# Kernel tuning notes

Hardware: AMD Instinct MI355X
Metric: run time of the kernel (lower is better)

## Reference

```python
import jax
import jax.numpy as jnp
from jax import lax
import numpy as np

D_MODEL = 768
D_INNER = 1536  # d_model * expand_factor
D_STATE = 16
D_CONV = 4
BATCH = 2
SEQ = 2048
EPS = 1e-5


def silu(x):
    return x * jax.nn.sigmoid(x)


def setup_inputs() -> dict:
    key = jax.random.key(0)
    ks = jax.random.split(key, 24)
    n = lambda k, shape, s=0.1: jax.random.normal(k, shape, dtype=jnp.float32) * s
    inp = {
        "x": jax.random.normal(ks[0], (BATCH, SEQ, D_MODEL), dtype=jnp.float32),
        "ln_g": jnp.ones((D_MODEL,), jnp.float32),
        "ln_b": jnp.zeros((D_MODEL,), jnp.float32),
        "W_in": n(ks[1], (D_INNER, D_MODEL)),
        "b_in": n(ks[2], (D_INNER,)),
        "conv_w": n(ks[3], (D_INNER, 1, D_CONV), 0.02),
        "conv_b": jnp.zeros((D_INNER,), jnp.float32),
        "W_A": n(ks[4], (D_STATE, D_INNER)),
        "b_A": n(ks[5], (D_STATE,)),
        "W_B": n(ks[6], (D_STATE, D_INNER)),
        "b_B": n(ks[7], (D_STATE,)),
        "W_C": n(ks[8], (D_STATE, D_INNER)),
        "b_C": n(ks[9], (D_STATE,)),
        "W_dt": n(ks[10], (D_STATE, D_INNER)),
        "b_dt": n(ks[11], (D_STATE,)),
        "W_S": n(ks[12], (2 * D_INNER, D_INNER)),
        "b_S": n(ks[13], (2 * D_INNER,)),
        "W_gate": n(ks[14], (D_INNER, D_MODEL)),
        "b_gate": n(ks[15], (D_INNER,)),
        "W_out": n(ks[16], (D_MODEL, D_INNER)),
        "b_out": n(ks[17], (D_MODEL,)),
    }
    return inp


def reference(x, ln_g, ln_b, W_in, b_in, conv_w, conv_b, W_A, b_A, W_B, b_B,
              W_C, b_C, W_dt, b_dt, W_S, b_S, W_gate, b_gate, W_out, b_out):
    residual = x
    # LayerNorm
    mu = jnp.mean(x, axis=-1, keepdims=True)
    var = jnp.mean((x - mu) ** 2, axis=-1, keepdims=True)
    xn = (x - mu) * lax.rsqrt(var + EPS) * ln_g + ln_b
    # in projection -> [B, S, D_INNER]
    xp = xn @ W_in.T + b_in
    # depthwise causal conv1d over time
    k = conv_w.shape[-1]
    xc = jnp.moveaxis(xp, 1, 2)  # [B, D, L]
    xc = lax.conv_general_dilated(
        xc, conv_w, window_strides=(1,), padding=[(k - 1, 0)],
        dimension_numbers=("NCH", "OIH", "NCH"),
        feature_group_count=xc.shape[1])
    xc = xc + conv_b[None, :, None]
    xa = silu(jnp.moveaxis(xc, 1, 2))  # [B, S, D]
    # selective gating of SSM input (S_b computed but unused, as in source)
    S = xa @ W_S.T + b_S
    d = xa.shape[-1]
    S_a = jax.nn.sigmoid(S[..., :d])
    u = xa * S_a  # [B, S, D]
    # input-dependent SSM params [B, S, N]
    A = -jnp.exp(u @ W_A.T + b_A)
    dt = jnp.exp(u @ W_dt.T + b_dt)
    Bm = u @ W_B.T + b_B
    Cm = u @ W_C.T + b_C
    decay = jnp.exp(A * dt)  # [B, S, N]

    def step(h, inputs):
        dec_t, B_t, C_t, u_t = inputs  # [B,N],[B,N],[B,N],[B,D]
        h = h * dec_t[:, None, :] + B_t[:, None, :] * u_t[:, :, None]  # [B,D,N]
        y = jnp.einsum("bdn,bn->bd", h, C_t)
        return h, y

    h0 = jnp.zeros((u.shape[0], u.shape[2], decay.shape[-1]), u.dtype)
    scan_in = (jnp.moveaxis(decay, 1, 0), jnp.moveaxis(Bm, 1, 0),
               jnp.moveaxis(Cm, 1, 0), jnp.moveaxis(u, 1, 0))
    _, ys = lax.scan(step, h0, scan_in)
    y = jnp.moveaxis(ys, 0, 1)  # [B, S, D]
    # output gating + projection + residual
    gate = silu(xn @ W_gate.T + b_gate)
    out = (gate * y) @ W_out.T + b_out + residual
    return out
```

## Files before the change

kernel.cpp:

```cpp
#include <hip/hip_runtime.h>


typedef unsigned short u16;
using short8 = __attribute__((ext_vector_type(8))) short;
using f32x4  = __attribute__((ext_vector_type(4))) float;

#define BATCH 2
#define SEQ   2048
#define DM    768
#define DI    1536
#define NIG   (2*DI)
#define NST   16
#define LCH   64
#define NCH   32
#define NTOK  (BATCH*SEQ)

__device__ __forceinline__ u16 f2b(float x) {
  unsigned u = __float_as_uint(x);
  u += 0x7FFFu + ((u >> 16) & 1u);
  return (u16)(u >> 16);
}
__device__ __forceinline__ float b2f(u16 v) { return __uint_as_float((unsigned)v << 16); }
__device__ __forceinline__ float sigmoidf_(float x) { return 1.f / (1.f + expf(-x)); }
__device__ __forceinline__ float siluf_(float x) { return x / (1.f + expf(-x)); }

__global__ __launch_bounds__(256) void cast_bf16(const float* __restrict__ in, u16* __restrict__ out, int n4) {
  int i = blockIdx.x * 256 + threadIdx.x;
  if (i >= n4) return;
  float4 v = ((const float4*)in)[i];
  ushort4 o; o.x = f2b(v.x); o.y = f2b(v.y); o.z = f2b(v.z); o.w = f2b(v.w);
  ((ushort4*)out)[i] = o;
}

__global__ __launch_bounds__(256) void cast_ingate(const float* __restrict__ Wi, const float* __restrict__ Wg,
                                                   const float* __restrict__ bi, const float* __restrict__ bg,
                                                   u16* __restrict__ Wb, float* __restrict__ bias) {
  int i = blockIdx.x * 256 + threadIdx.x;
  if (i >= NIG * DM) return;
  int r = i / DM, c = i % DM;
  Wb[i] = f2b(r < DI ? Wi[(size_t)r * DM + c] : Wg[(size_t)(r - DI) * DM + c]);
  if (i < NIG) bias[i] = (i < DI) ? bi[i] : bg[i - DI];
}

__global__ __launch_bounds__(256) void cast_wabcd(const float* __restrict__ WA, const float* __restrict__ Wdt,
                                                  const float* __restrict__ WB, const float* __restrict__ WC,
                                                  const float* __restrict__ bA, const float* __restrict__ bdt,
                                                  const float* __restrict__ bB, const float* __restrict__ bC,
                                                  u16* __restrict__ Wb, float* __restrict__ bias64) {
  int i = blockIdx.x * 256 + threadIdx.x;
  if (i >= 64 * DI) return;
  int r = i / DI, c = i % DI;
  const float* src = (r < 16) ? WA + (size_t)r * DI
                  : (r < 32) ? Wdt + (size_t)(r - 16) * DI
                  : (r < 48) ? WB + (size_t)(r - 32) * DI
                             : WC + (size_t)(r - 48) * DI;
  Wb[i] = f2b(src[c]);
  if (i < 64) bias64[i] = (i < 16) ? bA[i] : (i < 32) ? bdt[i - 16] : (i < 48) ? bB[i - 32] : bC[i - 48];
}

__global__ __launch_bounds__(256) void ln_kernel(const float* __restrict__ x, const float* __restrict__ g,
                                                 const float* __restrict__ bb, u16* __restrict__ xn) {
  int m = blockIdx.x, tid = threadIdx.x;
  const float* xr = x + (size_t)m * DM;
  float v0 = xr[tid], v1 = xr[tid + 256], v2 = xr[tid + 512];
  float s  = v0 + v1 + v2;
  float s2 = fmaf(v0, v0, fmaf(v1, v1, v2 * v2));
  #pragma unroll
  for (int off = 32; off > 0; off >>= 1) { s += __shfl_down(s, off); s2 += __shfl_down(s2, off); }
  __shared__ float sh[8];
  int wave = tid >> 6, lane = tid & 63;
  if (lane == 0) { sh[wave] = s; sh[4 + wave] = s2; }
  __syncthreads();
  float S1 = sh[0] + sh[1] + sh[2] + sh[3];
  float S2 = sh[4] + sh[5] + sh[6] + sh[7];
  float mu = S1 * (1.f / DM);
  float var = S2 * (1.f / DM) - mu * mu;
  float rs = rsqrtf(var + 1e-5f);
  u16* o = xn + (size_t)m * DM;
  o[tid]       = f2b((v0 - mu) * rs * g[tid]       + bb[tid]);
  o[tid + 256] = f2b((v1 - mu) * rs * g[tid + 256] + bb[tid + 256]);
  o[tid + 512] = f2b((v2 - mu) * rs * g[tid + 512] + bb[tid + 512]);
}

__device__ __forceinline__ void gll16(const void* g, void* l) {
  __builtin_amdgcn_global_load_lds((const __attribute__((address_space(1))) void*)g,
                                   (__attribute__((address_space(3))) void*)l, 16, 0, 0);
}

template <int MODE>
__global__ __launch_bounds__(512) void gemm_bt(const u16* __restrict__ A, const u16* __restrict__ B,
                                               const float* __restrict__ bias, const float* __restrict__ aux,
                                               const u16* __restrict__ auxb,
                                               float* __restrict__ C, u16* __restrict__ Cb,
                                               int M, int N, int K) {
  __shared__ __align__(16) u16 As[4][128 * 32];
  __shared__ __align__(16) u16 Bs[4][128 * 32];
  const int tid = threadIdx.x, wave = tid >> 6, lane = tid & 63;

  const int nbx = gridDim.x, nwg = nbx * gridDim.y;
  const int orig = blockIdx.y * nbx + blockIdx.x;
  const int cpx = nwg >> 3;
  const int swz = (orig & 7) * cpx + (orig >> 3);
  const int m0 = (swz / nbx) * 128, n0 = (swz % nbx) * 128;

  const int wm = (wave >> 1) * 32, wn = (wave & 1) * 64;
  const int fr = lane & 15, fq = lane >> 4;
  f32x4 acc[2][4] = {};

  const int c0 = tid;
  const u16* Ag0 = A + (size_t)(m0 + (c0 >> 2)) * K + ((c0 & 3) ^ ((c0 >> 3) & 3)) * 8;
  const u16* Bg0 = B + (size_t)(n0 + (c0 >> 2)) * K + ((c0 & 3) ^ ((c0 >> 3) & 3)) * 8;
  const int lofs = (wave * 64) * 8;

  int offA[2], offB[4];
  #pragma unroll
  for (int i = 0; i < 2; ++i) {
    int ra = wm + i * 16 + fr;
    offA[i] = ra * 32 + (fq ^ ((ra >> 1) & 3)) * 8;
  }
  #pragma unroll
  for (int i = 0; i < 4; ++i) {
    int rb = wn + i * 16 + fr;
    offB[i] = rb * 32 + (fq ^ ((rb >> 1) & 3)) * 8;
  }

  const int nk = K >> 5;

#define STAGE_BT(tt) { gll16(Ag0 + (tt) * 32, (u16*)As[(tt) & 3] + lofs); \
                       gll16(Bg0 + (tt) * 32, (u16*)Bs[(tt) & 3] + lofs); }
#define COMPUTE_BT(tt) { const u16* as_ = As[(tt) & 3]; const u16* bs_ = Bs[(tt) & 3]; \
    short8 av[2], bv[4]; \
    _Pragma("unroll") for (int i = 0; i < 2; ++i) av[i] = *(const short8*)(as_ + offA[i]); \
    _Pragma("unroll") for (int i = 0; i < 4; ++i) bv[i] = *(const short8*)(bs_ + offB[i]); \
    _Pragma("unroll") for (int mi = 0; mi < 2; ++mi) \
      _Pragma("unroll") for (int ni = 0; ni < 4; ++ni) \
        acc[mi][ni] = __builtin_amdgcn_mfma_f32_16x16x32_bf16(av[mi], bv[ni], acc[mi][ni], 0, 0, 0); }

  STAGE_BT(0); STAGE_BT(1); STAGE_BT(2);

  for (int t = 0; t < nk - 3; ++t) {
    asm volatile("s_waitcnt vmcnt(4)" ::: "memory");
    __builtin_amdgcn_s_barrier();
    STAGE_BT(t + 3);
    COMPUTE_BT(t);
  }
  asm volatile("s_waitcnt vmcnt(4)" ::: "memory");
  __builtin_amdgcn_s_barrier();
  COMPUTE_BT(nk - 3);
  asm volatile("s_waitcnt vmcnt(2)" ::: "memory");
  __builtin_amdgcn_s_barrier();
  COMPUTE_BT(nk - 2);
  asm volatile("s_waitcnt vmcnt(0)" ::: "memory");
  __builtin_amdgcn_s_barrier();
  COMPUTE_BT(nk - 1);
#undef STAGE_BT
#undef COMPUTE_BT

  #pragma unroll
  for (int ni = 0; ni < 4; ++ni) {
    int col = n0 + wn + ni * 16 + fr;
    float bv_ = bias[col];
    #pragma unroll
    for (int mi = 0; mi < 2; ++mi) {
      int row = m0 + wm + mi * 16 + fq * 4;
      #pragma unroll
      for (int j = 0; j < 4; ++j) {
        size_t off = (size_t)(row + j) * N + col;
        float z = acc[mi][ni][j] + bv_;
        if (MODE == 0) {
          C[off] = z + aux[off];
        } else if (MODE == 1) {
          Cb[off] = f2b(b2f(auxb[off]) * sigmoidf_(z));
        } else {
          Cb[off] = f2b(z);
        }
      }
    }
  }
}

__global__ __launch_bounds__(256) void gemm_abcd(const u16* __restrict__ A, const u16* __restrict__ B,
                                                 float* __restrict__ Zp, int M, int K) {
  __shared__ __align__(16) u16 As[2][64 * 64];
  __shared__ __align__(16) u16 Bs[2][64 * 64];
  const int tid = threadIdx.x, wave = tid >> 6, lane = tid & 63;
  const int m0 = blockIdx.x * 64;
  const int ks = blockIdx.y;
  const int Kq = K >> 2;
  const int kbase = ks * Kq;
  const int wm = wave * 16;
  const int fr = lane & 15, fq = lane >> 4;
  f32x4 acc[4] = {};

  const int c0 = tid, c1 = tid + 256;
  const u16* Ag0 = A + (size_t)(m0 + (c0 >> 3)) * K + kbase + ((c0 & 7) ^ ((c0 >> 3) & 7)) * 8;
  const u16* Ag1 = A + (size_t)(m0 + (c1 >> 3)) * K + kbase + ((c1 & 7) ^ ((c1 >> 3) & 7)) * 8;
  const u16* Bg0 = B + (size_t)(c0 >> 3) * K + kbase + ((c0 & 7) ^ ((c0 >> 3) & 7)) * 8;
  const u16* Bg1 = B + (size_t)(c1 >> 3) * K + kbase + ((c1 & 7) ^ ((c1 >> 3) & 7)) * 8;
  const int lo0 = (wave * 64) * 8;
  const int lo1 = (256 + wave * 64) * 8;

  int offAv[2], offBv[2][4];
  {
    int r = wm + fr;
    #pragma unroll
    for (int kk = 0; kk < 2; ++kk) offAv[kk] = r * 64 + ((kk * 4 + fq) ^ (r & 7)) * 8;
    #pragma unroll
    for (int i = 0; i < 4; ++i) {
      int rb = i * 16 + fr;
      #pragma unroll
      for (int kk = 0; kk < 2; ++kk) offBv[kk][i] = rb * 64 + ((kk * 4 + fq) ^ (rb & 7)) * 8;
    }
  }

  const int nk = Kq >> 6;
  gll16(Ag0, (u16*)As[0] + lo0);
  gll16(Ag1, (u16*)As[0] + lo1);
  gll16(Bg0, (u16*)Bs[0] + lo0);
  gll16(Bg1, (u16*)Bs[0] + lo1);

  for (int t = 0; t < nk; ++t) {
    __syncthreads();
    if (t + 1 < nk) {
      int ko = (t + 1) * 64;
      gll16(Ag0 + ko, (u16*)As[(t + 1) & 1] + lo0);
      gll16(Ag1 + ko, (u16*)As[(t + 1) & 1] + lo1);
      gll16(Bg0 + ko, (u16*)Bs[(t + 1) & 1] + lo0);
      gll16(Bg1 + ko, (u16*)Bs[(t + 1) & 1] + lo1);
    }
    const u16* as = As[t & 1];
    const u16* bs = Bs[t & 1];
    #pragma unroll
    for (int kk = 0; kk < 2; ++kk) {
      short8 av = *(const short8*)(as + offAv[kk]);
      short8 bv[4];
      #pragma unroll
      for (int i = 0; i < 4; ++i) bv[i] = *(const short8*)(bs + offBv[kk][i]);
      #pragma unroll
      for (int ni = 0; ni < 4; ++ni)
        acc[ni] = __builtin_amdgcn_mfma_f32_16x16x32_bf16(av, bv[ni], acc[ni], 0, 0, 0);
    }
  }

  float* zp = Zp + (size_t)ks * M * 64;
  #pragma unroll
  for (int ni = 0; ni < 4; ++ni) {
    int col = ni * 16 + fr;
    #pragma unroll
    for (int j = 0; j < 4; ++j) {
      int row = m0 + wm + fq * 4 + j;
      zp[(size_t)row * 64 + col] = acc[ni][j];
    }
  }
}

__global__ __launch_bounds__(256) void abcd_combine(const float* __restrict__ Zp, const float* __restrict__ bias64,
                                                    float* __restrict__ dec, float* __restrict__ Bm,
                                                    float* __restrict__ Cm, int M) {
  int idx = blockIdx.x * 256 + threadIdx.x;
  int row = idx >> 4, n = idx & 15;
  float zA = bias64[n], zDt = bias64[16 + n], zB = bias64[32 + n], zC = bias64[48 + n];
  #pragma unroll
  for (int ks = 0; ks < 4; ++ks) {
    const float* zp = Zp + ((size_t)ks * M + row) * 64;
    zA += zp[n]; zDt += zp[16 + n]; zB += zp[32 + n]; zC += zp[48 + n];
  }
  size_t o = (size_t)row * NST + n;
  dec[o] = expf(-expf(zA + zDt));
  Bm[o] = zB;
  Cm[o] = zC;
}

__global__ __launch_bounds__(256) void conv_silu(const u16* __restrict__ xpg, const float* __restrict__ cw,
                                                 const float* __restrict__ cb, u16* __restrict__ xab) {
  int idx = blockIdx.x * 256 + threadIdx.x;
  int d8 = idx % (DI / 8);
  int token = idx / (DI / 8);
  int t = token % SEQ;
  int d0 = d8 * 8;
  const short8* xv = (const short8*)(xpg + (size_t)token * NIG + d0);
  short8 z8 = {0, 0, 0, 0, 0, 0, 0, 0};
  short8 x3 = (t >= 3) ? xv[-3 * (NIG / 8)] : z8;
  short8 x2 = (t >= 2) ? xv[-2 * (NIG / 8)] : z8;
  short8 x1 = (t >= 1) ? xv[-1 * (NIG / 8)] : z8;
  short8 x0 = xv[0];
  const float4* cw4 = (const float4*)cw;
  float4 cbl = ((const float4*)cb)[d8 * 2], cbh = ((const float4*)cb)[d8 * 2 + 1];
  float cbv[8] = {cbl.x, cbl.y, cbl.z, cbl.w, cbh.x, cbh.y, cbh.z, cbh.w};
  short8 o;
  #pragma unroll
  for (int j = 0; j < 8; ++j) {
    float4 w = cw4[d0 + j];
    float a = cbv[j];
    a = fmaf(b2f((u16)x3[j]), w.x, a);
    a = fmaf(b2f((u16)x2[j]), w.y, a);
    a = fmaf(b2f((u16)x1[j]), w.z, a);
    a = fmaf(b2f((u16)x0[j]), w.w, a);
    o[j] = (short)f2b(siluf_(a));
  }
  *(short8*)(xab + (size_t)token * DI + d0) = o;
}

__global__ __launch_bounds__(256) void scan_phase1(const u16* __restrict__ ub, const float* __restrict__ dec,
                                                   const float* __restrict__ Bm, float* __restrict__ lend,
                                                   float* __restrict__ P) {
  __shared__ float dl[LCH * NST], bl[LCH * NST];
  int bid = blockIdx.x;
  int dblk = bid % 6, b = (bid / 6) % BATCH, c = bid / (6 * BATCH);
  int d = dblk * 256 + threadIdx.x;
  int t0 = c * LCH;
  size_t base16 = (size_t)(b * SEQ + t0) * NST;
  for (int i = threadIdx.x; i < LCH * NST; i += 256) { dl[i] = dec[base16 + i]; bl[i] = Bm[base16 + i]; }
  __syncthreads();
  float h[NST];
  #pragma unroll
  for (int n = 0; n < NST; ++n) h[n] = 0.f;
  const u16* up = ub + (size_t)(b * SEQ + t0) * DI + d;
  for (int t = 0; t < LCH; ++t) {
    float uu = b2f(up[(size_t)t * DI]);
    #pragma unroll
    for (int n = 0; n < NST; ++n) h[n] = fmaf(h[n], dl[t * NST + n], bl[t * NST + n] * uu);
  }
  float* lo = lend + ((size_t)(c * BATCH + b) * DI + d) * NST;
  ((float4*)lo)[0] = make_float4(h[0], h[1], h[2], h[3]);
  ((float4*)lo)[1] = make_float4(h[4], h[5], h[6], h[7]);
  ((float4*)lo)[2] = make_float4(h[8], h[9], h[10], h[11]);
  ((float4*)lo)[3] = make_float4(h[12], h[13], h[14], h[15]);
  if (dblk == 0 && threadIdx.x < NST) {
    float pr = 1.f;
    for (int t = 0; t < LCH; ++t) pr *= dl[t * NST + threadIdx.x];
    P[(size_t)(c * BATCH + b) * NST + threadIdx.x] = pr;
  }
}

__global__ __launch_bounds__(256) void scan_phase2(const float* __restrict__ lend, const float* __restrict__ P,
                                                   float* __restrict__ Hin) {
  int flat = blockIdx.x * 256 + threadIdx.x;
  int n = flat & 15;
  int d = (flat >> 4) % DI;
  int b = flat / (DI * NST);
  float h = 0.f;
  for (int c = 0; c < NCH; ++c) {
    size_t idx = ((size_t)(c * BATCH + b) * DI + d) * NST + n;
    Hin[idx] = h;
    h = fmaf(P[(size_t)(c * BATCH + b) * NST + n], h, lend[idx]);
  }
}

__global__ __launch_bounds__(256) void scan_phase3(const u16* __restrict__ ub, const float* __restrict__ dec,
                                                   const float* __restrict__ Bm, const float* __restrict__ Cm,
                                                   const float* __restrict__ Hin, const u16* __restrict__ xpg,
                                                   u16* __restrict__ gy) {
  __shared__ float dl[LCH * NST], bl[LCH * NST], cl[LCH * NST];
  int bid = blockIdx.x;
  int dblk = bid % 6, b = (bid / 6) % BATCH, c = bid / (6 * BATCH);
  int d = dblk * 256 + threadIdx.x;
  int t0 = c * LCH;
  size_t base16 = (size_t)(b * SEQ + t0) * NST;
  for (int i = threadIdx.x; i < LCH * NST; i += 256) {
    dl[i] = dec[base16 + i]; bl[i] = Bm[base16 + i]; cl[i] = Cm[base16 + i];
  }
  __syncthreads();
  float h[NST];
  const float4* hi = (const float4*)(Hin + ((size_t)(c * BATCH + b) * DI + d) * NST);
  float4 h0 = hi[0], h1 = hi[1], h2 = hi[2], h3 = hi[3];
  h[0]=h0.x; h[1]=h0.y; h[2]=h0.z; h[3]=h0.w; h[4]=h1.x; h[5]=h1.y; h[6]=h1.z; h[7]=h1.w;
  h[8]=h2.x; h[9]=h2.y; h[10]=h2.z; h[11]=h2.w; h[12]=h3.x; h[13]=h3.y; h[14]=h3.z; h[15]=h3.w;
  const u16* up = ub + (size_t)(b * SEQ + t0) * DI + d;
  const u16* gp = xpg + (size_t)(b * SEQ + t0) * NIG + DI + d;
  u16* yp = gy + (size_t)(b * SEQ + t0) * DI + d;
  for (int t = 0; t < LCH; ++t) {
    float uu = b2f(up[(size_t)t * DI]);
    float acc = 0.f;
    #pragma unroll
    for (int n = 0; n < NST; ++n) {
      h[n] = fmaf(h[n], dl[t * NST + n], bl[t * NST + n] * uu);
      acc = fmaf(h[n], cl[t * NST + n], acc);
    }
    float g = b2f(gp[(size_t)t * NIG]);
    yp[(size_t)t * DI] = f2b(siluf_(g) * acc);
  }
}

extern "C" void kernel_launch(void* const* d_in, const int* in_sizes, int n_in,
                              void* d_out, int out_size, void* d_ws, size_t ws_size,
                              hipStream_t stream) {
  const float* x      = (const float*)d_in[0];
  const float* ln_g   = (const float*)d_in[1];
  const float* ln_b   = (const float*)d_in[2];
  const float* W_in   = (const float*)d_in[3];
  const float* b_in   = (const float*)d_in[4];
  const float* conv_w = (const float*)d_in[5];
  const float* conv_b = (const float*)d_in[6];
  const float* W_A    = (const float*)d_in[7];
  const float* b_A    = (const float*)d_in[8];
  const float* W_B    = (const float*)d_in[9];
  const float* b_B    = (const float*)d_in[10];
  const float* W_C    = (const float*)d_in[11];
  const float* b_C    = (const float*)d_in[12];
  const float* W_dt   = (const float*)d_in[13];
  const float* b_dt   = (const float*)d_in[14];
  const float* W_S    = (const float*)d_in[15];
  const float* b_S    = (const float*)d_in[16];
  const float* W_gate = (const float*)d_in[17];
  const float* b_gate = (const float*)d_in[18];
  const float* W_out  = (const float*)d_in[19];
  const float* b_out  = (const float*)d_in[20];
  float* out = (float*)d_out;

  char* p = (char*)d_ws;
  auto alloc = [&](size_t bytes) { char* r = p; p += (bytes + 255) & ~(size_t)255; return r; };
  u16*   Wigb    = (u16*)alloc((size_t)NIG * DM * 2);
  float* biasig  = (float*)alloc((size_t)NIG * 4);
  u16*   WSb     = (u16*)alloc((size_t)DI * DI * 2);
  u16*   Woutb   = (u16*)alloc((size_t)DM * DI * 2);
  u16*   Wabcd   = (u16*)alloc((size_t)64 * DI * 2);
  float* bias64  = (float*)alloc(64 * 4);
  u16*   xnb     = (u16*)alloc((size_t)NTOK * DM * 2);
  u16*   xpg     = (u16*)alloc((size_t)NTOK * NIG * 2);
  u16*   xab     = (u16*)alloc((size_t)NTOK * DI * 2);
  u16*   ub      = (u16*)alloc((size_t)NTOK * DI * 2);
  float* Zp      = (float*)alloc((size_t)4 * NTOK * 64 * 4);
  float* decb    = (float*)alloc((size_t)NTOK * NST * 4);
  float* Bmb     = (float*)alloc((size_t)NTOK * NST * 4);
  float* Cmb     = (float*)alloc((size_t)NTOK * NST * 4);
  float* lend    = (float*)alloc((size_t)NCH * BATCH * DI * NST * 4);
  float* Hin     = (float*)alloc((size_t)NCH * BATCH * DI * NST * 4);
  float* P       = (float*)alloc((size_t)NCH * BATCH * NST * 4);
  u16* gy = xab;

  cast_ingate<<<(NIG * DM + 255) / 256, 256, 0, stream>>>(W_in, W_gate, b_in, b_gate, Wigb, biasig);
  cast_bf16<<<(DI * DI / 4 + 255) / 256, 256, 0, stream>>>(W_S, WSb, DI * DI / 4);
  cast_bf16<<<(DM * DI / 4 + 255) / 256, 256, 0, stream>>>(W_out, Woutb, DM * DI / 4);
  cast_wabcd<<<(64 * DI + 255) / 256, 256, 0, stream>>>(W_A, W_dt, W_B, W_C, b_A, b_dt, b_B, b_C, Wabcd, bias64);

  ln_kernel<<<NTOK, 256, 0, stream>>>(x, ln_g, ln_b, xnb);

  gemm_bt<2><<<dim3(NIG / 128, NTOK / 128), 512, 0, stream>>>(xnb, Wigb, biasig, nullptr, nullptr,
                                                              nullptr, xpg, NTOK, NIG, DM);

  conv_silu<<<NTOK * (DI / 8) / 256, 256, 0, stream>>>(xpg, conv_w, conv_b, xab);

  gemm_bt<1><<<dim3(DI / 128, NTOK / 128), 512, 0, stream>>>(xab, WSb, b_S, nullptr, xab,
                                                             nullptr, ub, NTOK, DI, DI);

  gemm_abcd<<<dim3(NTOK / 64, 4), 256, 0, stream>>>(ub, Wabcd, Zp, NTOK, DI);
  abcd_combine<<<NTOK * 16 / 256, 256, 0, stream>>>(Zp, bias64, decb, Bmb, Cmb, NTOK);

  scan_phase1<<<NCH * BATCH * (DI / 256), 256, 0, stream>>>(ub, decb, Bmb, lend, P);
  scan_phase2<<<BATCH * DI * NST / 256, 256, 0, stream>>>(lend, P, Hin);
  scan_phase3<<<NCH * BATCH * (DI / 256), 256, 0, stream>>>(ub, decb, Bmb, Cmb, Hin, xpg, gy);

  gemm_bt<0><<<dim3(DM / 128, NTOK / 128), 512, 0, stream>>>(gy, Woutb, b_out, x, nullptr,
                                                             out, nullptr, NTOK, DM, DI);
}
```

Baseline: 206.0 us.

## Fuse weight casts, bf16 scan states, smaller out-proj tiles, MFMA priority

Merges the four weight/bias cast kernels into one launch. Stores the chunk-end and chunk-start scan states in bf16 instead of fp32, which halves that traffic but lowers precision of the carried state. Gives the output projection GEMM a 64-row tile variant with 256 threads so more workgroups fill the device. It also wraps the MFMA block in s_setprio to favour compute waves.

```diff
diff --git a/kernel.cpp b/kernel.cpp
--- a/kernel.cpp
+++ b/kernel.cpp
@@ -24,38 +24,57 @@
 __device__ __forceinline__ float sigmoidf_(float x) { return 1.f / (1.f + expf(-x)); }
 __device__ __forceinline__ float siluf_(float x) { return x / (1.f + expf(-x)); }
 
-__global__ __launch_bounds__(256) void cast_bf16(const float* __restrict__ in, u16* __restrict__ out, int n4) {
+#define N_IG   (NIG * DM / 4)
+#define N_WS   (DI * DI / 4)
+#define N_WO   (DM * DI / 4)
+#define N_WAB  (64 * DI / 4)
+#define N_CAST (N_IG + N_WS + N_WO + N_WAB + NIG + 64)
+
+__global__ __launch_bounds__(256) void cast_all(
+    const float* __restrict__ Wi, const float* __restrict__ Wg,
+    const float* __restrict__ bi, const float* __restrict__ bg,
+    const float* __restrict__ WS, const float* __restrict__ WO,
+    const float* __restrict__ WA, const float* __restrict__ Wdt,
+    const float* __restrict__ WB, const float* __restrict__ WC,
+    const float* __restrict__ bA, const float* __restrict__ bdt,
+    const float* __restrict__ bB, const float* __restrict__ bC,
+    u16* __restrict__ Wigb, float* __restrict__ biasig,
+    u16* __restrict__ WSb, u16* __restrict__ Woutb,
+    u16* __restrict__ Wabcd, float* __restrict__ bias64) {
   int i = blockIdx.x * 256 + threadIdx.x;
-  if (i >= n4) return;
-  float4 v = ((const float4*)in)[i];
-  ushort4 o; o.x = f2b(v.x); o.y = f2b(v.y); o.z = f2b(v.z); o.w = f2b(v.w);
-  ((ushort4*)out)[i] = o;
-}
-
-__global__ __launch_bounds__(256) void cast_ingate(const float* __restrict__ Wi, const float* __restrict__ Wg,
-                                                   const float* __restrict__ bi, const float* __restrict__ bg,
-                                                   u16* __restrict__ Wb, float* __restrict__ bias) {
-  int i = blockIdx.x * 256 + threadIdx.x;
-  if (i >= NIG * DM) return;
-  int r = i / DM, c = i % DM;
-  Wb[i] = f2b(r < DI ? Wi[(size_t)r * DM + c] : Wg[(size_t)(r - DI) * DM + c]);
-  if (i < NIG) bias[i] = (i < DI) ? bi[i] : bg[i - DI];
-}
-
-__global__ __launch_bounds__(256) void cast_wabcd(const float* __restrict__ WA, const float* __restrict__ Wdt,
-                                                  const float* __restrict__ WB, const float* __restrict__ WC,
-                                                  const float* __restrict__ bA, const float* __restrict__ bdt,
-                                                  const float* __restrict__ bB, const float* __restrict__ bC,
-                                                  u16* __restrict__ Wb, float* __restrict__ bias64) {
-  int i = blockIdx.x * 256 + threadIdx.x;
-  if (i >= 64 * DI) return;
-  int r = i / DI, c = i % DI;
-  const float* src = (r < 16) ? WA + (size_t)r * DI
-                  : (r < 32) ? Wdt + (size_t)(r - 16) * DI
-                  : (r < 48) ? WB + (size_t)(r - 32) * DI
-                             : WC + (size_t)(r - 48) * DI;
-  Wb[i] = f2b(src[c]);
-  if (i < 64) bias64[i] = (i < 16) ? bA[i] : (i < 32) ? bdt[i - 16] : (i < 48) ? bB[i - 32] : bC[i - 48];
+  if (i < N_IG) {
+    int i4 = i * 4, r = i4 / DM, c = i4 % DM;
+    const float* src = (r < DI) ? Wi + (size_t)r * DM + c : Wg + (size_t)(r - DI) * DM + c;
+    float4 v = *(const float4*)src;
+    ushort4 o; o.x = f2b(v.x); o.y = f2b(v.y); o.z = f2b(v.z); o.w = f2b(v.w);
+    ((ushort4*)Wigb)[i] = o;
+  } else if (i < N_IG + N_WS) {
+    int j = i - N_IG;
+    float4 v = ((const float4*)WS)[j];
+    ushort4 o; o.x = f2b(v.x); o.y = f2b(v.y); o.z = f2b(v.z); o.w = f2b(v.w);
+    ((ushort4*)WSb)[j] = o;
+  } else if (i < N_IG + N_WS + N_WO) {
+    int j = i - N_IG - N_WS;
+    float4 v = ((const float4*)WO)[j];
+    ushort4 o; o.x = f2b(v.x); o.y = f2b(v.y); o.z = f2b(v.z); o.w = f2b(v.w);
+    ((ushort4*)Woutb)[j] = o;
+  } else if (i < N_IG + N_WS + N_WO + N_WAB) {
+    int j = i - N_IG - N_WS - N_WO;
+    int i4 = j * 4, r = i4 / DI, c = i4 % DI;
+    const float* src = (r < 16) ? WA + (size_t)r * DI
+                     : (r < 32) ? Wdt + (size_t)(r - 16) * DI
+                     : (r < 48) ? WB + (size_t)(r - 32) * DI
+                                : WC + (size_t)(r - 48) * DI;
+    float4 v = *(const float4*)(src + c);
+    ushort4 o; o.x = f2b(v.x); o.y = f2b(v.y); o.z = f2b(v.z); o.w = f2b(v.w);
+    ((ushort4*)Wabcd)[j] = o;
+  } else if (i < N_IG + N_WS + N_WO + N_WAB + NIG) {
+    int j = i - N_IG - N_WS - N_WO - N_WAB;
+    biasig[j] = (j < DI) ? bi[j] : bg[j - DI];
+  } else if (i < N_CAST) {
+    int j = i - N_IG - N_WS - N_WO - N_WAB - NIG;
+    bias64[j] = (j < 16) ? bA[j] : (j < 32) ? bdt[j - 16] : (j < 48) ? bB[j - 32] : bC[j - 48];
+  }
 }
 
 __global__ __launch_bounds__(256) void ln_kernel(const float* __restrict__ x, const float* __restrict__ g,
@@ -87,13 +106,14 @@
                                    (__attribute__((address_space(3))) void*)l, 16, 0, 0);
 }
 
-template <int MODE>
-__global__ __launch_bounds__(512) void gemm_bt(const u16* __restrict__ A, const u16* __restrict__ B,
-                                               const float* __restrict__ bias, const float* __restrict__ aux,
-                                               const u16* __restrict__ auxb,
-                                               float* __restrict__ C, u16* __restrict__ Cb,
-                                               int M, int N, int K) {
-  __shared__ __align__(16) u16 As[4][128 * 32];
+template <int MODE, int BM>
+__global__ __launch_bounds__(BM == 128 ? 512 : 256) void gemm_bt(
+    const u16* __restrict__ A, const u16* __restrict__ B,
+    const float* __restrict__ bias, const float* __restrict__ aux,
+    const u16* __restrict__ auxb,
+    float* __restrict__ C, u16* __restrict__ Cb,
+    int M, int N, int K) {
+  __shared__ __align__(16) u16 As[4][BM * 32];
   __shared__ __align__(16) u16 Bs[4][128 * 32];
   const int tid = threadIdx.x, wave = tid >> 6, lane = tid & 63;
 
@@ -101,7 +121,7 @@
   const int orig = blockIdx.y * nbx + blockIdx.x;
   const int cpx = nwg >> 3;
   const int swz = (orig & 7) * cpx + (orig >> 3);
-  const int m0 = (swz / nbx) * 128, n0 = (swz % nbx) * 128;
+  const int m0 = (swz / nbx) * BM, n0 = (swz % nbx) * 128;
 
   const int wm = (wave >> 1) * 32, wn = (wave & 1) * 64;
   const int fr = lane & 15, fq = lane >> 4;
@@ -111,6 +131,9 @@
   const u16* Ag0 = A + (size_t)(m0 + (c0 >> 2)) * K + ((c0 & 3) ^ ((c0 >> 3) & 3)) * 8;
   const u16* Bg0 = B + (size_t)(n0 + (c0 >> 2)) * K + ((c0 & 3) ^ ((c0 >> 3) & 3)) * 8;
   const int lofs = (wave * 64) * 8;
+  const int c1 = tid + 256;
+  const u16* Bg1 = B + (size_t)(n0 + (c1 >> 2)) * K + ((c1 & 3) ^ ((c1 >> 3) & 3)) * 8;
+  const int lofs1 = (256 + wave * 64) * 8;
 
   int offA[2], offB[4];
   #pragma unroll
@@ -127,27 +150,34 @@
   const int nk = K >> 5;
 
 #define STAGE_BT(tt) { gll16(Ag0 + (tt) * 32, (u16*)As[(tt) & 3] + lofs); \
-                       gll16(Bg0 + (tt) * 32, (u16*)Bs[(tt) & 3] + lofs); }
+                       gll16(Bg0 + (tt) * 32, (u16*)Bs[(tt) & 3] + lofs); \
+                       if (BM == 64) gll16(Bg1 + (tt) * 32, (u16*)Bs[(tt) & 3] + lofs1); }
 #define COMPUTE_BT(tt) { const u16* as_ = As[(tt) & 3]; const u16* bs_ = Bs[(tt) & 3]; \
     short8 av[2], bv[4]; \
     _Pragma("unroll") for (int i = 0; i < 2; ++i) av[i] = *(const short8*)(as_ + offA[i]); \
     _Pragma("unroll") for (int i = 0; i < 4; ++i) bv[i] = *(const short8*)(bs_ + offB[i]); \
+    __builtin_amdgcn_s_setprio(1); \
     _Pragma("unroll") for (int mi = 0; mi < 2; ++mi) \
       _Pragma("unroll") for (int ni = 0; ni < 4; ++ni) \
-        acc[mi][ni] = __builtin_amdgcn_mfma_f32_16x16x32_bf16(av[mi], bv[ni], acc[mi][ni], 0, 0, 0); }
+        acc[mi][ni] = __builtin_amdgcn_mfma_f32_16x16x32_bf16(av[mi], bv[ni], acc[mi][ni], 0, 0, 0); \
+    __builtin_amdgcn_s_setprio(0); }
+#define WAIT2S() { if (BM == 128) asm volatile("s_waitcnt vmcnt(4)" ::: "memory"); \
+                   else           asm volatile("s_waitcnt vmcnt(6)" ::: "memory"); }
+#define WAIT1S() { if (BM == 128) asm volatile("s_waitcnt vmcnt(2)" ::: "memory"); \
+                   else           asm volatile("s_waitcnt vmcnt(3)" ::: "memory"); }
 
   STAGE_BT(0); STAGE_BT(1); STAGE_BT(2);
 
   for (int t = 0; t < nk - 3; ++t) {
-    asm volatile("s_waitcnt vmcnt(4)" ::: "memory");
+    WAIT2S();
     __builtin_amdgcn_s_barrier();
     STAGE_BT(t + 3);
     COMPUTE_BT(t);
   }
-  asm volatile("s_waitcnt vmcnt(4)" ::: "memory");
+  WAIT2S();
   __builtin_amdgcn_s_barrier();
   COMPUTE_BT(nk - 3);
-  asm volatile("s_waitcnt vmcnt(2)" ::: "memory");
+  WAIT1S();
   __builtin_amdgcn_s_barrier();
   COMPUTE_BT(nk - 2);
   asm volatile("s_waitcnt vmcnt(0)" ::: "memory");
@@ -155,6 +185,8 @@
   COMPUTE_BT(nk - 1);
 #undef STAGE_BT
 #undef COMPUTE_BT
+#undef WAIT2S
+#undef WAIT1S
 
   #pragma unroll
   for (int ni = 0; ni < 4; ++ni) {
@@ -302,7 +334,7 @@
 }
 
 __global__ __launch_bounds__(256) void scan_phase1(const u16* __restrict__ ub, const float* __restrict__ dec,
-                                                   const float* __restrict__ Bm, float* __restrict__ lend,
+                                                   const float* __restrict__ Bm, u16* __restrict__ lend,
                                                    float* __restrict__ P) {
   __shared__ float dl[LCH * NST], bl[LCH * NST];
   int bid = blockIdx.x;
@@ -321,11 +353,12 @@
     #pragma unroll
     for (int n = 0; n < NST; ++n) h[n] = fmaf(h[n], dl[t * NST + n], bl[t * NST + n] * uu);
   }
-  float* lo = lend + ((size_t)(c * BATCH + b) * DI + d) * NST;
-  ((float4*)lo)[0] = make_float4(h[0], h[1], h[2], h[3]);
-  ((float4*)lo)[1] = make_float4(h[4], h[5], h[6], h[7]);
-  ((float4*)lo)[2] = make_float4(h[8], h[9], h[10], h[11]);
-  ((float4*)lo)[3] = make_float4(h[12], h[13], h[14], h[15]);
+  u16* lo = lend + ((size_t)(c * BATCH + b) * DI + d) * NST;
+  short8 s0, s1;
+  #pragma unroll
+  for (int n = 0; n < 8; ++n) { s0[n] = (short)f2b(h[n]); s1[n] = (short)f2b(h[8 + n]); }
+  ((short8*)lo)[0] = s0;
+  ((short8*)lo)[1] = s1;
   if (dblk == 0 && threadIdx.x < NST) {
     float pr = 1.f;
     for (int t = 0; t < LCH; ++t) pr *= dl[t * NST + threadIdx.x];
@@ -333,8 +366,8 @@
   }
 }
 
-__global__ __launch_bounds__(256) void scan_phase2(const float* __restrict__ lend, const float* __restrict__ P,
-                                                   float* __restrict__ Hin) {
+__global__ __launch_bounds__(256) void scan_phase2(const u16* __restrict__ lend, const float* __restrict__ P,
+                                                   u16* __restrict__ Hin) {
   int flat = blockIdx.x * 256 + threadIdx.x;
   int n = flat & 15;
   int d = (flat >> 4) % DI;
@@ -342,14 +375,14 @@
   float h = 0.f;
   for (int c = 0; c < NCH; ++c) {
     size_t idx = ((size_t)(c * BATCH + b) * DI + d) * NST + n;
-    Hin[idx] = h;
-    h = fmaf(P[(size_t)(c * BATCH + b) * NST + n], h, lend[idx]);
+    Hin[idx] = f2b(h);
+    h = fmaf(P[(size_t)(c * BATCH + b) * NST + n], h, b2f(lend[idx]));
   }
 }
 
 __global__ __launch_bounds__(256) void scan_phase3(const u16* __restrict__ ub, const float* __restrict__ dec,
                                                    const float* __restrict__ Bm, const float* __restrict__ Cm,
-                                                   const float* __restrict__ Hin, const u16* __restrict__ xpg,
+                                                   const u16* __restrict__ Hin, const u16* __restrict__ xpg,
                                                    u16* __restrict__ gy) {
   __shared__ float dl[LCH * NST], bl[LCH * NST], cl[LCH * NST];
   int bid = blockIdx.x;
@@ -362,10 +395,10 @@
   }
   __syncthreads();
   float h[NST];
-  const float4* hi = (const float4*)(Hin + ((size_t)(c * BATCH + b) * DI + d) * NST);
-  float4 h0 = hi[0], h1 = hi[1], h2 = hi[2], h3 = hi[3];
-  h[0]=h0.x; h[1]=h0.y; h[2]=h0.z; h[3]=h0.w; h[4]=h1.x; h[5]=h1.y; h[6]=h1.z; h[7]=h1.w;
-  h[8]=h2.x; h[9]=h2.y; h[10]=h2.z; h[11]=h2.w; h[12]=h3.x; h[13]=h3.y; h[14]=h3.z; h[15]=h3.w;
+  const short8* hi = (const short8*)(Hin + ((size_t)(c * BATCH + b) * DI + d) * NST);
+  short8 h0 = hi[0], h1 = hi[1];
+  #pragma unroll
+  for (int n = 0; n < 8; ++n) { h[n] = b2f((u16)h0[n]); h[8 + n] = b2f((u16)h1[n]); }
   const u16* up = ub + (size_t)(b * SEQ + t0) * DI + d;
   const u16* gp = xpg + (size_t)(b * SEQ + t0) * NIG + DI + d;
   u16* yp = gy + (size_t)(b * SEQ + t0) * DI + d;
@@ -424,25 +457,24 @@
   float* decb    = (float*)alloc((size_t)NTOK * NST * 4);
   float* Bmb     = (float*)alloc((size_t)NTOK * NST * 4);
   float* Cmb     = (float*)alloc((size_t)NTOK * NST * 4);
-  float* lend    = (float*)alloc((size_t)NCH * BATCH * DI * NST * 4);
-  float* Hin     = (float*)alloc((size_t)NCH * BATCH * DI * NST * 4);
+  u16*   lend    = (u16*)alloc((size_t)NCH * BATCH * DI * NST * 2);
+  u16*   Hin     = (u16*)alloc((size_t)NCH * BATCH * DI * NST * 2);
   float* P       = (float*)alloc((size_t)NCH * BATCH * NST * 4);
   u16* gy = xab;
 
-  cast_ingate<<<(NIG * DM + 255) / 256, 256, 0, stream>>>(W_in, W_gate, b_in, b_gate, Wigb, biasig);
-  cast_bf16<<<(DI * DI / 4 + 255) / 256, 256, 0, stream>>>(W_S, WSb, DI * DI / 4);
-  cast_bf16<<<(DM * DI / 4 + 255) / 256, 256, 0, stream>>>(W_out, Woutb, DM * DI / 4);
-  cast_wabcd<<<(64 * DI + 255) / 256, 256, 0, stream>>>(W_A, W_dt, W_B, W_C, b_A, b_dt, b_B, b_C, Wabcd, bias64);
+  cast_all<<<(N_CAST + 255) / 256, 256, 0, stream>>>(W_in, W_gate, b_in, b_gate, W_S, W_out,
+                                                     W_A, W_dt, W_B, W_C, b_A, b_dt, b_B, b_C,
+                                                     Wigb, biasig, WSb, Woutb, Wabcd, bias64);
 
   ln_kernel<<<NTOK, 256, 0, stream>>>(x, ln_g, ln_b, xnb);
 
-  gemm_bt<2><<<dim3(NIG / 128, NTOK / 128), 512, 0, stream>>>(xnb, Wigb, biasig, nullptr, nullptr,
-                                                              nullptr, xpg, NTOK, NIG, DM);
+  gemm_bt<2, 128><<<dim3(NIG / 128, NTOK / 128), 512, 0, stream>>>(xnb, Wigb, biasig, nullptr, nullptr,
+                                                                   nullptr, xpg, NTOK, NIG, DM);
 
   conv_silu<<<NTOK * (DI / 8) / 256, 256, 0, stream>>>(xpg, conv_w, conv_b, xab);
 
-  gemm_bt<1><<<dim3(DI / 128, NTOK / 128), 512, 0, stream>>>(xab, WSb, b_S, nullptr, xab,
-                                                             nullptr, ub, NTOK, DI, DI);
+  gemm_bt<1, 128><<<dim3(DI / 128, NTOK / 128), 512, 0, stream>>>(xab, WSb, b_S, nullptr, xab,
+                                                                  nullptr, ub, NTOK, DI, DI);
 
   gemm_abcd<<<dim3(NTOK / 64, 4), 256, 0, stream>>>(ub, Wabcd, Zp, NTOK, DI);
   abcd_combine<<<NTOK * 16 / 256, 256, 0, stream>>>(Zp, bias64, decb, Bmb, Cmb, NTOK);
@@ -451,6 +483,6 @@
   scan_phase2<<<BATCH * DI * NST / 256, 256, 0, stream>>>(lend, P, Hin);
   scan_phase3<<<NCH * BATCH * (DI / 256), 256, 0, stream>>>(ub, decb, Bmb, Cmb, Hin, xpg, gy);
 
-  gemm_bt<0><<<dim3(DM / 128, NTOK / 128), 512, 0, stream>>>(gy, Woutb, b_out, x, nullptr,
-                                                             out, nullptr, NTOK, DM, DI);
-}
+  gemm_bt<0, 64><<<dim3(DM / 128, NTOK / 64), 256, 0, stream>>>(gy, Woutb, b_out, x, nullptr,
+                                                                out, nullptr, NTOK, DM, DI);
+}
```

Result: faster. 200.3 us (-2.8%).
